# Performance work log

Hardware: AMD Instinct MI355X
Metric: run time of the kernel (lower is better)

## Reference

```python
import jax, jax.numpy as jnp
import numpy as np

V, DS, DF, H, NPASS = 32000, 64, 256, 8, 2
B, L, NB = 2, 1024, 512
EPS = 1e-5


def setup_inputs() -> dict:
    ks = jax.random.split(jax.random.key(0), 20)
    def n(k, shape, scale=0.02):
        return (scale * jax.random.normal(k, shape)).astype(jnp.float32)
    return {
        "token_ids": jax.random.randint(ks[0], (B, L), 0, V),
        "tok_mu": n(ks[1], (V, DS)),
        "tok_log_var": n(ks[2], (V, DS)),
        "tok_raw_alpha": n(ks[3], (V, 1), 1.0),
        "tok_features": n(ks[4], (V, DF)),
        "pos_mu": n(ks[5], (L, DS)),
        "qproj_w": n(ks[6], (H * DS, DS)),
        "qproj_b": jnp.zeros((H * DS,), jnp.float32),
        "hproj_w": n(ks[7], (DF, H * DF)),
        "hproj_b": jnp.zeros((DF,), jnp.float32),
        "mu_up_w": n(ks[8], (DS, 2 * DF)),
        "mu_up_b": jnp.zeros((DS,), jnp.float32),
        "agate_w": n(ks[9], (1, 2 * DF)),
        "agate_b": jnp.zeros((1,), jnp.float32),
        "ffn_w": n(ks[10], (DF, 2 * DF)),
        "ffn_b": jnp.zeros((DF,), jnp.float32),
        "ln_g": jnp.ones((DF,), jnp.float32),
        "ln_b": jnp.zeros((DF,), jnp.float32),
        "lm_w": n(ks[11], (V, DF)),
        "lm_b": jnp.zeros((V,), jnp.float32),
        "blob_mu": n(ks[12], (NB, DS)),
        "blob_lv": n(ks[13], (NB, DS)),
        "blob_ra": n(ks[14], (NB,), 1.0),
        "blob_f": n(ks[15], (NB, DF)),
        "bgate_w": n(ks[16], (1, 2 * DF)),
        "bgate_b": jnp.zeros((1,), jnp.float32),
    }


def _composite_weights(a):
    # front-to-back alpha compositing along last axis: w_j = a_j * prod_{k<j}(1-a_k)
    T = jnp.cumprod(1.0 - a, axis=-1)
    T_ex = jnp.concatenate([jnp.ones_like(T[..., :1]), T[..., :-1]], axis=-1)
    return a * T_ex, T[..., -1]


def _forward(token_ids, tok_mu, tok_log_var, tok_raw_alpha, tok_features, pos_mu,
             qproj_w, qproj_b, hproj_w, hproj_b, mu_up_w, mu_up_b, agate_w, agate_b,
             ffn_w, ffn_b, ln_g, ln_b, lm_w, lm_b, blob_mu, blob_lv, blob_ra, blob_f,
             bgate_w, bgate_b):
    Bc, Lc = token_ids.shape
    mu = tok_mu[token_ids] + pos_mu[:Lc][None]          # [B,L,DS]
    log_var = tok_log_var[token_ids]                     # [B,L,DS]
    alpha = jax.nn.sigmoid(tok_raw_alpha[token_ids][..., 0])  # [B,L]
    features = tok_features[token_ids]                   # [B,L,DF]

    # ---- blob query + blob render ----
    query = mu.mean(axis=1)                              # [B,DS]
    iv_b = jnp.exp(-blob_lv)                             # [NB,DS]
    d2b = (jnp.einsum('bd,nd->bn', query * query, iv_b)
           - 2.0 * jnp.einsum('bd,nd->bn', query, blob_mu * iv_b)
           + jnp.sum(blob_mu * blob_mu * iv_b, -1)[None])
    Kb = jnp.exp(-0.5 * d2b)                             # [B,NB]
    ab = jax.nn.sigmoid(blob_ra)[None] * Kb              # effective alpha
    wb, t_residual = _composite_weights(ab)
    blob_meaning = jnp.einsum('bn,nf->bf', wb, blob_f)   # [B,DF] (blob_proj = Identity)

    # ---- word meaning: multi-pass Gaussian causal render ----
    mask = jnp.tril(jnp.ones((Lc, Lc), jnp.float32))
    iv = jnp.exp(-log_var)                               # inv-variance, fixed across passes
    cur_mu, cur_alpha, cur_feat = mu, alpha, features
    meaning = None
    for p in range(NPASS):
        q = (cur_mu @ qproj_w.T + qproj_b).reshape(Bc, Lc, H, DS).transpose(0, 2, 1, 3)  # [B,H,L,DS]
        # squared Mahalanobis distance via three GEMM-style contractions (no [B,H,L,L,DS] tensor)
        d2 = (jnp.einsum('bhid,bjd->bhij', q * q, iv)
              - 2.0 * jnp.einsum('bhid,bjd->bhij', q, cur_mu * iv)
              + jnp.sum(cur_mu * cur_mu * iv, -1)[:, None, None, :])
        K = jnp.exp(-0.5 * d2)                           # [B,H,L,L]
        a = cur_alpha[:, None, None, :] * K * mask
        w, _ = _composite_weights(a)
        m = jnp.einsum('bhij,bjf->bhif', w, cur_feat)    # [B,H,L,DF]
        m_cat = m.transpose(0, 2, 1, 3).reshape(Bc, Lc, H * DF)
        meaning = m_cat @ hproj_w.T + hproj_b            # [B,L,DF] (dropout = eval/identity)
        if p < NPASS - 1:
            ctx = jnp.concatenate([cur_feat, meaning], axis=-1)  # [B,L,2DF]
            cur_mu = cur_mu + ctx @ mu_up_w.T + mu_up_b
            cur_alpha = cur_alpha * jax.nn.sigmoid(ctx @ agate_w.T + agate_b)[..., 0]
            cur_feat = cur_feat + ctx @ ffn_w.T + ffn_b

    # ---- blob gate fusion ----
    blob_exp = jnp.broadcast_to(blob_meaning[:, None, :], meaning.shape)
    gate = jax.nn.sigmoid(jnp.concatenate([blob_exp, meaning], -1) @ bgate_w.T + bgate_b)  # [B,L,1]
    t_res = t_residual[:, None, None]
    fused = (1.0 - t_res) * gate * blob_exp + t_res * meaning

    # ---- final layernorm + lm head ----
    mean = fused.mean(-1, keepdims=True)
    var = ((fused - mean) ** 2).mean(-1, keepdims=True)
    h = (fused - mean) * jax.lax.rsqrt(var + EPS) * ln_g + ln_b
    logits = h @ lm_w.T + lm_b                           # [B,L,V]
    return logits


def reference(token_ids, tok_mu, tok_log_var, tok_raw_alpha, tok_features, pos_mu,
              qproj_w, qproj_b, hproj_w, hproj_b, mu_up_w, mu_up_b, agate_w, agate_b,
              ffn_w, ffn_b, ln_g, ln_b, lm_w, lm_b, blob_mu, blob_lv, blob_ra, blob_f,
              bgate_w, bgate_b):
    return _forward(token_ids, tok_mu, tok_log_var, tok_raw_alpha, tok_features, pos_mu,
                    qproj_w, qproj_b, hproj_w, hproj_b, mu_up_w, mu_up_b, agate_w, agate_b,
                    ffn_w, ffn_b, ln_g, ln_b, lm_w, lm_b, blob_mu, blob_lv, blob_ra, blob_f,
                    bgate_w, bgate_b)
```

## Files before the change

### kernel.cpp

```cpp
#include <hip/hip_runtime.h>
#include <hip/hip_bf16.h>
#include <cstdint>
#include <cstddef>

#define V_   32000
#define DS_  64
#define DF_  256
#define H_   8
#define L_   1024
#define B_   2
#define NB_  512
#define BL_  2048
#define EPS_ 1e-5f

typedef unsigned short ushort_t;
typedef unsigned int uint_t;
typedef short bf16x8 __attribute__((ext_vector_type(8)));
typedef float f32x4 __attribute__((ext_vector_type(4)));
#define AS1 __attribute__((address_space(1)))
#define AS3 __attribute__((address_space(3)))

__device__ __forceinline__ float sigmoidf_(float x) { return 1.f / (1.f + __expf(-x)); }
__device__ __forceinline__ ushort_t f2bf(float x) {
    __hip_bfloat16 b = __float2bfloat16(x);
    return __builtin_bit_cast(ushort_t, b);
}
__device__ __forceinline__ uint_t packbf(float lo, float hi) {
    return ((uint_t)f2bf(hi) << 16) | (uint_t)f2bf(lo);
}
__device__ __forceinline__ float bflo(uint_t v) {
    return __builtin_bit_cast(float, v << 16);
}
__device__ __forceinline__ float bfhi(uint_t v) {
    return __builtin_bit_cast(float, v & 0xFFFF0000u);
}

__device__ __forceinline__ float block_reduce_sum(float v, float* red) {
    int t = threadIdx.x;
    red[t] = v;
    __syncthreads();
    for (int s = 128; s > 0; s >>= 1) {
        if (t < s) red[t] += red[t + s];
        __syncthreads();
    }
    float r = red[0];
    __syncthreads();
    return r;
}

#define NCVT_ 8720
#define NGA_  (NCVT_ + BL_)
#define NST_  (NGA_ + B_)
__global__ __launch_bounds__(256) void k_setup(
    const int* __restrict__ tok, const float* __restrict__ tok_mu,
    const float* __restrict__ tok_lv, const float* __restrict__ tok_ra,
    const float* __restrict__ tok_f, const float* __restrict__ pos_mu,
    const float* __restrict__ qproj_w, const float* __restrict__ mu_up_w,
    const float* __restrict__ mu_up_b, const float* __restrict__ ffn_w,
    const float* __restrict__ ffn_b, const float* __restrict__ agate_w,
    const float* __restrict__ agate_b, const float* __restrict__ hproj_w,
    const float* __restrict__ lm_w, const float* __restrict__ blob_mu,
    const float* __restrict__ blob_lv, const float* __restrict__ blob_ra,
    const float* __restrict__ blob_f,
    ushort_t* __restrict__ qpwbf, ushort_t* __restrict__ cwbf,
    ushort_t* __restrict__ hpwbf, ushort_t* __restrict__ wbf,
    float* __restrict__ cbias,
    float* __restrict__ mu, ushort_t* __restrict__ mub16,
    uint_t* __restrict__ muivP, float* __restrict__ alpha,
    float* __restrict__ feat, ushort_t* __restrict__ featb16,
    ushort_t* __restrict__ fTg, float* __restrict__ blobm,
    float* __restrict__ tres) {
    int blk = blockIdx.x;
    int t = threadIdx.x;
    if (blk < 32) {
        int i = (blk * 256 + t) * 4;
        float4 v = *reinterpret_cast<const float4*>(qproj_w + i);
        ushort4 o = {f2bf(v.x), f2bf(v.y), f2bf(v.z), f2bf(v.w)};
        *reinterpret_cast<ushort4*>(qpwbf + i) = o;
        return;
    }
    if (blk < 208) {
        int i = ((blk - 32) * 256 + t) * 4;
        int r = i >> 9, c = i & 511;
        float4 v = {0.f, 0.f, 0.f, 0.f};
        if (r < 64)        v = *reinterpret_cast<const float4*>(mu_up_w + r * 512 + c);
        else if (r < 320)  v = *reinterpret_cast<const float4*>(ffn_w + (r - 64) * 512 + c);
        else if (r == 320) v = *reinterpret_cast<const float4*>(agate_w + c);
        ushort4 o = {f2bf(v.x), f2bf(v.y), f2bf(v.z), f2bf(v.w)};
        *reinterpret_cast<ushort4*>(cwbf + i) = o;
        return;
    }
    if (blk < 720) {
        int i = ((blk - 208) * 256 + t) * 4;
        float4 v = *reinterpret_cast<const float4*>(hproj_w + i);
        ushort4 o = {f2bf(v.x), f2bf(v.y), f2bf(v.z), f2bf(v.w)};
        *reinterpret_cast<ushort4*>(hpwbf + i) = o;
        return;
    }
    if (blk < NCVT_) {
        int i = ((blk - 720) * 256 + t) * 4;
        float4 v = *reinterpret_cast<const float4*>(lm_w + i);
        ushort4 o = {f2bf(v.x), f2bf(v.y), f2bf(v.z), f2bf(v.w)};
        *reinterpret_cast<ushort4*>(wbf + i) = o;
        return;
    }
    if (blk < NGA_) {
        int row = blk - NCVT_;
        int l = row & (L_ - 1);
        int v = tok[row];
        if (t < DS_) {
            float m = tok_mu[(size_t)v * DS_ + t] + pos_mu[l * DS_ + t];
            mu[(size_t)row * DS_ + t] = m;
            mub16[(size_t)row * DS_ + t] = f2bf(m);
            float ivv = __expf(-tok_lv[(size_t)v * DS_ + t]);
            muivP[(size_t)t * BL_ + row] = packbf(m, ivv);
        }
        float fv = tok_f[(size_t)v * DF_ + t];
        feat[(size_t)row * DF_ + t] = fv;
        featb16[(size_t)row * DF_ + t] = f2bf(fv);
        int jb = (l >> 3) & 7, jr = l & 7;
        int jp = (l & ~63) | ((jb ^ (t & 7)) << 3) | jr;
        fTg[((size_t)((row >> 10) * DF_ + t) << 10) + jp] = f2bf(fv);
        if (t == 0) alpha[row] = sigmoidf_(tok_ra[v]);
        return;
    }
    if (blk < NST_) {
        __shared__ float red[256];
        __shared__ int stok[L_];
        __shared__ float sq[DS_];
        __shared__ float sa[NB_];
        __shared__ float sp[NB_];
        int b = blk - NGA_;
        for (int l = t; l < L_; l += 256) stok[l] = tok[b * L_ + l];
        __syncthreads();
        int d = t & 63, c = t >> 6;
        float s = 0.f;
        for (int l = c; l < L_; l += 4)
            s += tok_mu[(size_t)stok[l] * DS_ + d] + pos_mu[l * DS_ + d];
        red[t] = s;
        __syncthreads();
        if (c == 0)
            sq[d] = (red[d] + red[64 + d] + red[128 + d] + red[192 + d]) * (1.f / L_);
        __syncthreads();
        for (int n = t; n < NB_; n += 256) {
            float d2 = 0.f;
            for (int dd = 0; dd < DS_; ++dd) {
                float diff = sq[dd] - blob_mu[n * DS_ + dd];
                d2 += __expf(-blob_lv[n * DS_ + dd]) * diff * diff;
            }
            float a = sigmoidf_(blob_ra[n]) * __expf(-0.5f * d2);
            sa[n] = a;
            sp[n] = 1.f - a;
        }
        __syncthreads();
        int n0 = t, n1 = t + 256;
        for (int s2 = 1; s2 < NB_; s2 <<= 1) {
            float t0 = (n0 >= s2) ? sp[n0 - s2] : 1.f;
            float t1 = (n1 >= s2) ? sp[n1 - s2] : 1.f;
            __syncthreads();
            sp[n0] *= t0;
            sp[n1] *= t1;
            __syncthreads();
        }
        float w0 = sa[n0] * (n0 ? sp[n0 - 1] : 1.f);
        float w1 = sa[n1] * sp[n1 - 1];
        __syncthreads();
        sa[n0] = w0;
        sa[n1] = w1;
        if (t == 0) tres[b] = sp[NB_ - 1];
        __syncthreads();
        float acc = 0.f;
        for (int n = 0; n < NB_; ++n) acc += sa[n] * blob_f[n * DF_ + t];
        blobm[b * DF_ + t] = acc;
        return;
    }
    for (int idx = t; idx < 352; idx += 256) {
        float bv = 0.f;
        if (idx < 64) bv = mu_up_b[idx];
        else if (idx < 320) bv = ffn_b[idx - 64];
        else if (idx == 320) bv = agate_b[0];
        cbias[idx] = bv;
    }
}

__global__ __launch_bounds__(512) void k_attn5(
    const float* __restrict__ q, const uint_t* __restrict__ muivP,
    const float* __restrict__ alpha, const ushort_t* __restrict__ fTg,
    ushort_t* __restrict__ mcatb) {
    __shared__ __align__(16) uint_t smiu[64 * 64];
    __shared__ __align__(16) ushort_t sfT[256 * 64];
    __shared__ __align__(16) ushort_t sw16[16][72];
    __shared__ float sq[H_][64];
    __shared__ float sT[H_];
    int tid = threadIdx.x;
    int w = tid >> 6, lane = tid & 63;
    int bid = blockIdx.x;
    int b = bid >> 10, i = bid & (L_ - 1);
    int row = b * L_ + i;
    const int lr = lane & 15, q4 = lane >> 4;

    for (int k = tid; k < 16 * 72; k += 512) ((ushort_t*)sw16)[k] = 0;
    sq[w][lane] = q[(size_t)row * 512 + tid];

    float T = 1.f;
    f32x4 acc0 = {}, acc1 = {};

    for (int j0 = 0; j0 <= i; j0 += 64) {
        __syncthreads();
        if (j0 > 0) {
            bool alive = false;
            #pragma unroll
            for (int h = 0; h < H_; ++h) alive |= (sT[h] >= 1e-12f);
            if (!alive) break;
        }
        {
            const uint_t* src = muivP + b * L_ + j0;
            #pragma unroll
            for (int r = 0; r < 2; ++r) {
                int d = w * 8 + r * 4 + q4;
                const uint_t* gp = src + (size_t)d * BL_ + lr * 4;
                __builtin_amdgcn_global_load_lds((const AS1 uint_t*)gp,
                    (AS3 uint_t*)&smiu[(w * 8 + r * 4) * 64], 16, 0, 0);
            }
        }
        {
            #pragma unroll
            for (int it = 0; it < 4; ++it) {
                int c0 = w * 32 + it * 8;
                const ushort_t* gp = fTg +
                    ((size_t)(b * DF_ + c0 + (lane >> 3)) << 10) + j0 + (lane & 7) * 8;
                __builtin_amdgcn_global_load_lds((const AS1 uint_t*)gp,
                    (AS3 uint_t*)&sfT[c0 * 64], 16, 0, 0);
            }
        }
        __syncthreads();

        int jj = j0 + lane;
        float d2a = 0.f;
        #pragma unroll 8
        for (int d = 0; d < 64; ++d) {
            uint_t v = smiu[d * 64 + lane];
            float m = bflo(v), iv = bfhi(v);
            float diff = sq[w][d] - m;
            d2a = fmaf(iv * diff, diff, d2a);
        }
        float a = (jj <= i) ? alpha[b * L_ + jj] * __expf(-0.5f * d2a) : 0.f;

        float p = 1.f - a;
        #pragma unroll
        for (int s = 1; s < 64; s <<= 1) {
            float tt = __shfl_up(p, s, 64);
            if (lane >= s) p *= tt;
        }
        float Tex = __shfl_up(p, 1, 64);
        if (lane == 0) Tex = 1.f;
        sw16[w][lane] = f2bf(a * T * Tex);
        float Tch = __shfl(p, 63, 64);
        T *= Tch;
        if (lane == 0) sT[w] = T;
        __syncthreads();

        #pragma unroll
        for (int kk = 0; kk < 2; ++kk) {
            bf16x8 afr = *reinterpret_cast<const bf16x8*>(
                (const char*)sw16 + lr * 144 + kk * 64 + q4 * 16);
            {
                int c = (w * 2 + 0) * 16 + lr;
                int bo = c * 128 + ((kk * 64 + q4 * 16) ^ ((c & 7) << 4));
                bf16x8 bfr = *reinterpret_cast<const bf16x8*>((const char*)sfT + bo);
                acc0 = __builtin_amdgcn_mfma_f32_16x16x32_bf16(afr, bfr, acc0, 0, 0, 0);
            }
            {
                int c = (w * 2 + 1) * 16 + lr;
                int bo = c * 128 + ((kk * 64 + q4 * 16) ^ ((c & 7) << 4));
                bf16x8 bfr = *reinterpret_cast<const bf16x8*>((const char*)sfT + bo);
                acc1 = __builtin_amdgcn_mfma_f32_16x16x32_bf16(afr, bfr, acc1, 0, 0, 0);
            }
        }
    }
    if (q4 < 2) {
        #pragma unroll
        for (int r = 0; r < 4; ++r) {
            int h = q4 * 4 + r;
            int c0 = (w * 2 + 0) * 16 + lr;
            int c1 = (w * 2 + 1) * 16 + lr;
            mcatb[(size_t)row * 2048 + h * 256 + c0] = f2bf(acc0[r]);
            mcatb[(size_t)row * 2048 + h * 256 + c1] = f2bf(acc1[r]);
        }
    }
}

template <int BM, int BN, int BK, int WGM, int WGN, bool NTS, bool WB16>
__global__ __launch_bounds__(256) void gemm_mfma2(
    const ushort_t* __restrict__ A, const ushort_t* __restrict__ A2, int K1,
    int strideA, const ushort_t* __restrict__ W, const float* __restrict__ bias,
    float* __restrict__ C, ushort_t* __restrict__ Cb, int M, int N, int K) {
    constexpr int WMF = BM / WGM / 16;
    constexpr int WNF = BN / WGN / 16;
    constexpr int KK  = BK / 32;
    constexpr int AHALF = BM * BK;
    constexpr int BHALF = BN * BK;
    constexpr int STAGE_B = 2 * (AHALF + BHALF) * 2;
    constexpr int EPI_B = BM * BN * 4;
    constexpr int SMEM_B = STAGE_B > EPI_B ? STAGE_B : EPI_B;
    __shared__ __align__(16) char smem[SMEM_B];
    ushort_t* As = (ushort_t*)smem;
    ushort_t* Bs = (ushort_t*)(smem + 2 * AHALF * 2);

    const int tid = threadIdx.x;
    const int wave = tid >> 6, lane = tid & 63;
    const int m0 = blockIdx.x * BM, n0 = blockIdx.y * BN;
    const int wr = wave / WGN, wc = wave % WGN;
    const int lr = lane & 15;
    const int q4 = lane >> 4;

    f32x4 acc[WMF][WNF] = {};

    auto stage = [&](int buf, int t) {
        const int k0g = t * BK;
        const ushort_t* Abase = (A2 != nullptr && k0g >= K1) ? A2 : A;
        const int kof = (A2 != nullptr && k0g >= K1) ? k0g - K1 : k0g;
        ushort_t* Ad = As + buf * AHALF;
        #pragma unroll
        for (int it = 0; it < (BM * BK / 8) / 256; ++it) {
            int cbase = it * 256 + wave * 64;
            int c = cbase + lane;
            int r = c & (BM - 1), c8 = c / BM;
            const ushort_t* gp = Abase + (size_t)(m0 + r) * strideA + kof + c8 * 8;
            __builtin_amdgcn_global_load_lds((const AS1 uint_t*)gp,
                                             (AS3 uint_t*)(Ad + cbase * 8), 16, 0, 0);
        }
        ushort_t* Bd = Bs + buf * BHALF;
        #pragma unroll
        for (int it = 0; it < (BN * BK / 8) / 256; ++it) {
            int cbase = it * 256 + wave * 64;
            int c = cbase + lane;
            int r = c & (BN - 1), c8 = c / BN;
            const ushort_t* gp = W + (size_t)(n0 + r) * K + k0g + c8 * 8;
            __builtin_amdgcn_global_load_lds((const AS1 uint_t*)gp,
                                             (AS3 uint_t*)(Bd + cbase * 8), 16, 0, 0);
        }
    };

    const int nsteps = K / BK;
    stage(0, 0);
    __syncthreads();
    for (int t = 0; t < nsteps; ++t) {
        const int cur = t & 1;
        if (t + 1 < nsteps) stage(cur ^ 1, t + 1);
        const ushort_t* Ab = As + cur * AHALF;
        const ushort_t* Bb = Bs + cur * BHALF;
        bf16x8 af[WMF][KK], bfr[WNF][KK];
        #pragma unroll
        for (int mi = 0; mi < WMF; ++mi)
            #pragma unroll
            for (int kk = 0; kk < KK; ++kk)
                af[mi][kk] = *reinterpret_cast<const bf16x8*>(
                    &Ab[((kk * 4 + q4) * BM + wr * (BM / WGM) + mi * 16 + lr) * 8]);
        #pragma unroll
        for (int ni = 0; ni < WNF; ++ni)
            #pragma unroll
            for (int kk = 0; kk < KK; ++kk)
                bfr[ni][kk] = *reinterpret_cast<const bf16x8*>(
                    &Bb[((kk * 4 + q4) * BN + wc * (BN / WGN) + ni * 16 + lr) * 8]);
        #pragma unroll
        for (int kk = 0; kk < KK; ++kk)
            #pragma unroll
            for (int mi = 0; mi < WMF; ++mi)
                #pragma unroll
                for (int ni = 0; ni < WNF; ++ni)
                    acc[mi][ni] = __builtin_amdgcn_mfma_f32_16x16x32_bf16(
                        af[mi][kk], bfr[ni][kk], acc[mi][ni], 0, 0, 0);
        __syncthreads();
    }

    float* tile = (float*)smem;
    #pragma unroll
    for (int mi = 0; mi < WMF; ++mi)
        #pragma unroll
        for (int ni = 0; ni < WNF; ++ni) {
            int col = wc * (BN / WGN) + ni * 16 + lr;
            float bv = bias[n0 + col];
            #pragma unroll
            for (int j = 0; j < 4; ++j) {
                int r2 = wr * (BM / WGM) + mi * 16 + q4 * 4 + j;
                tile[r2 * BN + col] = acc[mi][ni][j] + bv;
            }
        }
    __syncthreads();
    constexpr int EV = (BM * BN / 4) / 256;
    #pragma unroll
    for (int e = 0; e < EV; ++e) {
        int idx = e * 256 + tid;
        int r = idx / (BN / 4), c4 = idx % (BN / 4);
        f32x4 v = reinterpret_cast<const f32x4*>(tile)[idx];
        f32x4* dst = reinterpret_cast<f32x4*>(&C[(size_t)(m0 + r) * N + n0 + c4 * 4]);
        if (NTS) __builtin_nontemporal_store(v, dst);
        else *dst = v;
        if (WB16) {
            ushort4 ob = {f2bf(v[0]), f2bf(v[1]), f2bf(v[2]), f2bf(v[3])};
            *reinterpret_cast<ushort4*>(&Cb[(size_t)(m0 + r) * N + n0 + c4 * 4]) = ob;
        }
    }
}

__global__ __launch_bounds__(256) void k_apply(
    const float* __restrict__ dctx, float* __restrict__ mu,
    ushort_t* __restrict__ mub16, uint_t* __restrict__ muivP,
    float* __restrict__ alpha, float* __restrict__ feat,
    ushort_t* __restrict__ featb16, ushort_t* __restrict__ fTg) {
    int row = blockIdx.x, t = threadIdx.x;
    int l = row & (L_ - 1);
    const float* dr = dctx + (size_t)row * 352;
    if (t == 0) alpha[row] *= sigmoidf_(dr[320]);
    if (t < DS_) {
        float m = mu[(size_t)row * DS_ + t] + dr[t];
        mu[(size_t)row * DS_ + t] = m;
        mub16[(size_t)row * DS_ + t] = f2bf(m);
        uint_t v = muivP[(size_t)t * BL_ + row];
        muivP[(size_t)t * BL_ + row] = (v & 0xFFFF0000u) | (uint_t)f2bf(m);
    }
    float fn = feat[(size_t)row * DF_ + t] + dr[64 + t];
    feat[(size_t)row * DF_ + t] = fn;
    featb16[(size_t)row * DF_ + t] = f2bf(fn);
    int jb = (l >> 3) & 7, jr = l & 7;
    int jp = (l & ~63) | ((jb ^ (t & 7)) << 3) | jr;
    fTg[((size_t)((row >> 10) * DF_ + t) << 10) + jp] = f2bf(fn);
}

__global__ __launch_bounds__(256) void k_fused_ln(
    const float* __restrict__ meaning, const float* __restrict__ blobm,
    const float* __restrict__ tres, const float* __restrict__ bgw,
    const float* __restrict__ bgb, const float* __restrict__ ln_g,
    const float* __restrict__ ln_b, ushort_t* __restrict__ houtb) {
    __shared__ float red[256];
    int row = blockIdx.x, t = threadIdx.x;
    int b = row >> 10;
    float m = meaning[(size_t)row * DF_ + t];
    float be = blobm[b * DF_ + t];
    float tr = tres[b];
    float gsum = block_reduce_sum(be * bgw[t] + m * bgw[256 + t], red);
    float gate = sigmoidf_(gsum + bgb[0]);
    float f = (1.f - tr) * gate * be + tr * m;
    float mean = block_reduce_sum(f, red) * (1.f / DF_);
    float d = f - mean;
    float var = block_reduce_sum(d * d, red) * (1.f / DF_);
    houtb[(size_t)row * DF_ + t] = f2bf(d * rsqrtf(var + EPS_) * ln_g[t] + ln_b[t]);
}

extern "C" void kernel_launch(void* const* d_in, const int* in_sizes, int n_in,
                              void* d_out, int out_size, void* d_ws, size_t ws_size,
                              hipStream_t stream) {
    const int*   tok      = (const int*)d_in[0];
    const float* tok_mu   = (const float*)d_in[1];
    const float* tok_lv   = (const float*)d_in[2];
    const float* tok_ra   = (const float*)d_in[3];
    const float* tok_f    = (const float*)d_in[4];
    const float* pos_mu   = (const float*)d_in[5];
    const float* qproj_w  = (const float*)d_in[6];
    const float* qproj_b  = (const float*)d_in[7];
    const float* hproj_w  = (const float*)d_in[8];
    const float* hproj_b  = (const float*)d_in[9];
    const float* mu_up_w  = (const float*)d_in[10];
    const float* mu_up_b  = (const float*)d_in[11];
    const float* agate_w  = (const float*)d_in[12];
    const float* agate_b  = (const float*)d_in[13];
    const float* ffn_w    = (const float*)d_in[14];
    const float* ffn_b    = (const float*)d_in[15];
    const float* ln_g     = (const float*)d_in[16];
    const float* ln_b     = (const float*)d_in[17];
    const float* lm_w     = (const float*)d_in[18];
    const float* lm_b     = (const float*)d_in[19];
    const float* blob_mu  = (const float*)d_in[20];
    const float* blob_lv  = (const float*)d_in[21];
    const float* blob_ra  = (const float*)d_in[22];
    const float* blob_f   = (const float*)d_in[23];
    const float* bgate_w  = (const float*)d_in[24];
    const float* bgate_b  = (const float*)d_in[25];
    float* out = (float*)d_out;

    float* ws = (float*)d_ws;
    float* mu      = ws;
    float* alpha   = mu + BL_ * DS_;
    float* feat    = alpha + BL_;
    float* blobm   = feat + BL_ * DF_;
    float* tres    = blobm + B_ * DF_;
    float* q       = tres + 64;
    float* meaning = q + BL_ * 512;
    float* dctx    = meaning + BL_ * DF_;
    float* cbias   = dctx + (size_t)BL_ * 352;
    uint_t* muivP  = (uint_t*)(cbias + 384);
    ushort_t* fTg   = (ushort_t*)(muivP + (size_t)DS_ * BL_);
    ushort_t* mub16 = fTg + (size_t)B_ * DF_ * L_;
    ushort_t* featb16 = mub16 + (size_t)BL_ * DS_;
    ushort_t* meanb16 = featb16 + (size_t)BL_ * DF_;
    ushort_t* mcatb = meanb16 + (size_t)BL_ * DF_;
    ushort_t* hbufb = mcatb + (size_t)BL_ * 2048;
    ushort_t* wbf   = hbufb + (size_t)BL_ * DF_;
    ushort_t* hpwbf = wbf + (size_t)V_ * DF_;
    ushort_t* qpwbf = hpwbf + (size_t)DF_ * 2048;
    ushort_t* cwbf  = qpwbf + (size_t)512 * 64;

    k_setup<<<NST_ + 1, 256, 0, stream>>>(
        tok, tok_mu, tok_lv, tok_ra, tok_f, pos_mu,
        qproj_w, mu_up_w, mu_up_b, ffn_w, ffn_b, agate_w, agate_b,
        hproj_w, lm_w, blob_mu, blob_lv, blob_ra, blob_f,
        qpwbf, cwbf, hpwbf, wbf, cbias,
        mu, mub16, muivP, alpha, feat, featb16, fTg, blobm, tres);

    for (int p = 0; p < 2; ++p) {
        gemm_mfma2<32, 32, 64, 2, 2, false, false>
            <<<dim3(BL_ / 32, 512 / 32), 256, 0, stream>>>(
            mub16, nullptr, 0, DS_, qpwbf, qproj_b, q, nullptr, BL_, 512, DS_);
        k_attn5<<<BL_, 512, 0, stream>>>(q, muivP, alpha, fTg, mcatb);
        if (p == 0) {
            gemm_mfma2<32, 32, 128, 2, 2, false, true>
                <<<dim3(BL_ / 32, DF_ / 32), 256, 0, stream>>>(
                mcatb, nullptr, 0, H_ * DF_, hpwbf, hproj_b, meaning, meanb16,
                BL_, DF_, H_ * DF_);
            gemm_mfma2<32, 32, 128, 2, 2, false, false>
                <<<dim3(BL_ / 32, 352 / 32), 256, 0, stream>>>(
                featb16, meanb16, DF_, DF_, cwbf, cbias, dctx, nullptr,
                BL_, 352, 512);
            k_apply<<<BL_, 256, 0, stream>>>(dctx, mu, mub16, muivP, alpha,
                                             feat, featb16, fTg);
        } else {
            gemm_mfma2<32, 32, 128, 2, 2, false, false>
                <<<dim3(BL_ / 32, DF_ / 32), 256, 0, stream>>>(
                mcatb, nullptr, 0, H_ * DF_, hpwbf, hproj_b, meaning, nullptr,
                BL_, DF_, H_ * DF_);
        }
    }

    k_fused_ln<<<BL_, 256, 0, stream>>>(meaning, blobm, tres, bgate_w, bgate_b,
                                        ln_g, ln_b, hbufb);
    gemm_mfma2<128, 128, 64, 2, 2, true, false>
        <<<dim3(BL_ / 128, V_ / 128), 256, 0, stream>>>(
        hbufb, nullptr, 0, DF_, wbf, lm_b, out, nullptr, BL_, V_, DF_);
}
```

Measured before the change: 312.0 us.

## Process two query rows per attention block, coarsen setup conversion, shrink LM-head tile

The attention kernel now handles two adjacent query rows per block, so the loaded mu/inv-var and feature tiles are shared and the 16 MFMA A-rows are fully used instead of half. The setup kernel converts four float4 chunks per thread, which cuts the number of conversion blocks by four. The LM-head GEMM tile changes from 128x128 to 64x128 to launch more workgroups. The costs are a second per-row scan, more registers, and the block only exits early once both rows are saturated.

```diff
diff --git a/kernel.cpp b/kernel.cpp
--- a/kernel.cpp
+++ b/kernel.cpp
@@ -48,7 +48,7 @@
     return r;
 }
 
-#define NCVT_ 8720
+#define NCVT_ 2180
 #define NGA_  (NCVT_ + BL_)
 #define NST_  (NGA_ + B_)
 __global__ __launch_bounds__(256) void k_setup(
@@ -72,36 +72,27 @@
     float* __restrict__ tres) {
     int blk = blockIdx.x;
     int t = threadIdx.x;
-    if (blk < 32) {
-        int i = (blk * 256 + t) * 4;
-        float4 v = *reinterpret_cast<const float4*>(qproj_w + i);
-        ushort4 o = {f2bf(v.x), f2bf(v.y), f2bf(v.z), f2bf(v.w)};
-        *reinterpret_cast<ushort4*>(qpwbf + i) = o;
-        return;
-    }
-    if (blk < 208) {
-        int i = ((blk - 32) * 256 + t) * 4;
-        int r = i >> 9, c = i & 511;
-        float4 v = {0.f, 0.f, 0.f, 0.f};
-        if (r < 64)        v = *reinterpret_cast<const float4*>(mu_up_w + r * 512 + c);
-        else if (r < 320)  v = *reinterpret_cast<const float4*>(ffn_w + (r - 64) * 512 + c);
-        else if (r == 320) v = *reinterpret_cast<const float4*>(agate_w + c);
-        ushort4 o = {f2bf(v.x), f2bf(v.y), f2bf(v.z), f2bf(v.w)};
-        *reinterpret_cast<ushort4*>(cwbf + i) = o;
-        return;
-    }
-    if (blk < 720) {
-        int i = ((blk - 208) * 256 + t) * 4;
-        float4 v = *reinterpret_cast<const float4*>(hproj_w + i);
-        ushort4 o = {f2bf(v.x), f2bf(v.y), f2bf(v.z), f2bf(v.w)};
-        *reinterpret_cast<ushort4*>(hpwbf + i) = o;
-        return;
-    }
     if (blk < NCVT_) {
-        int i = ((blk - 720) * 256 + t) * 4;
-        float4 v = *reinterpret_cast<const float4*>(lm_w + i);
-        ushort4 o = {f2bf(v.x), f2bf(v.y), f2bf(v.z), f2bf(v.w)};
-        *reinterpret_cast<ushort4*>(wbf + i) = o;
+        const float* s = nullptr; ushort_t* dd; int base; bool cw = false;
+        if (blk < 8)        { s = qproj_w; dd = qpwbf; base = blk; }
+        else if (blk < 52)  { dd = cwbf; base = blk - 8; cw = true; }
+        else if (blk < 180) { s = hproj_w; dd = hpwbf; base = blk - 52; }
+        else                { s = lm_w; dd = wbf; base = blk - 180; }
+        #pragma unroll
+        for (int k = 0; k < 4; ++k) {
+            int i = base * 4096 + k * 1024 + t * 4;
+            float4 v = {0.f, 0.f, 0.f, 0.f};
+            if (cw) {
+                int r = i >> 9, c = i & 511;
+                if (r < 64)        v = *reinterpret_cast<const float4*>(mu_up_w + r * 512 + c);
+                else if (r < 320)  v = *reinterpret_cast<const float4*>(ffn_w + (r - 64) * 512 + c);
+                else if (r == 320) v = *reinterpret_cast<const float4*>(agate_w + c);
+            } else {
+                v = *reinterpret_cast<const float4*>(s + i);
+            }
+            ushort4 o = {f2bf(v.x), f2bf(v.y), f2bf(v.z), f2bf(v.w)};
+            *reinterpret_cast<ushort4*>(dd + i) = o;
+        }
         return;
     }
     if (blk < NGA_) {
@@ -183,34 +174,35 @@
     }
 }
 
-__global__ __launch_bounds__(512) void k_attn5(
+__global__ __launch_bounds__(512) void k_attn7(
     const float* __restrict__ q, const uint_t* __restrict__ muivP,
     const float* __restrict__ alpha, const ushort_t* __restrict__ fTg,
     ushort_t* __restrict__ mcatb) {
     __shared__ __align__(16) uint_t smiu[64 * 64];
     __shared__ __align__(16) ushort_t sfT[256 * 64];
     __shared__ __align__(16) ushort_t sw16[16][72];
-    __shared__ float sq[H_][64];
-    __shared__ float sT[H_];
+    __shared__ float sqA[512], sqB[512];
+    __shared__ float sT[16];
     int tid = threadIdx.x;
     int w = tid >> 6, lane = tid & 63;
     int bid = blockIdx.x;
-    int b = bid >> 10, i = bid & (L_ - 1);
-    int row = b * L_ + i;
+    int b = bid >> 9;
+    int i0 = (bid & 511) * 2, i1 = i0 + 1;
+    int row0 = b * L_ + i0;
     const int lr = lane & 15, q4 = lane >> 4;
 
-    for (int k = tid; k < 16 * 72; k += 512) ((ushort_t*)sw16)[k] = 0;
-    sq[w][lane] = q[(size_t)row * 512 + tid];
-
-    float T = 1.f;
+    sqA[tid] = q[(size_t)row0 * 512 + tid];
+    sqB[tid] = q[(size_t)(row0 + 1) * 512 + tid];
+
+    float T0 = 1.f, T1 = 1.f;
     f32x4 acc0 = {}, acc1 = {};
 
-    for (int j0 = 0; j0 <= i; j0 += 64) {
+    for (int j0 = 0; j0 <= i1; j0 += 64) {
         __syncthreads();
         if (j0 > 0) {
             bool alive = false;
             #pragma unroll
-            for (int h = 0; h < H_; ++h) alive |= (sT[h] >= 1e-12f);
+            for (int h = 0; h < 16; ++h) alive |= (sT[h] >= 1e-12f);
             if (!alive) break;
         }
         {
@@ -236,17 +228,22 @@
         __syncthreads();
 
         int jj = j0 + lane;
-        float d2a = 0.f;
+        int jc = jj <= i1 ? jj : i1;
+        float alv = alpha[b * L_ + jc];
+        float d20 = 0.f, d21 = 0.f;
         #pragma unroll 8
         for (int d = 0; d < 64; ++d) {
             uint_t v = smiu[d * 64 + lane];
             float m = bflo(v), iv = bfhi(v);
-            float diff = sq[w][d] - m;
-            d2a = fmaf(iv * diff, diff, d2a);
-        }
-        float a = (jj <= i) ? alpha[b * L_ + jj] * __expf(-0.5f * d2a) : 0.f;
-
-        float p = 1.f - a;
+            float f0 = sqA[w * 64 + d] - m;
+            float f1 = sqB[w * 64 + d] - m;
+            d20 = fmaf(iv * f0, f0, d20);
+            d21 = fmaf(iv * f1, f1, d21);
+        }
+        float a0 = (jj <= i0) ? alv * __expf(-0.5f * d20) : 0.f;
+        float a1 = (jj <= i1) ? alv * __expf(-0.5f * d21) : 0.f;
+
+        float p = 1.f - a0;
         #pragma unroll
         for (int s = 1; s < 64; s <<= 1) {
             float tt = __shfl_up(p, s, 64);
@@ -254,10 +251,21 @@
         }
         float Tex = __shfl_up(p, 1, 64);
         if (lane == 0) Tex = 1.f;
-        sw16[w][lane] = f2bf(a * T * Tex);
-        float Tch = __shfl(p, 63, 64);
-        T *= Tch;
-        if (lane == 0) sT[w] = T;
+        sw16[w][lane] = f2bf(a0 * T0 * Tex);
+        T0 *= __shfl(p, 63, 64);
+
+        p = 1.f - a1;
+        #pragma unroll
+        for (int s = 1; s < 64; s <<= 1) {
+            float tt = __shfl_up(p, s, 64);
+            if (lane >= s) p *= tt;
+        }
+        Tex = __shfl_up(p, 1, 64);
+        if (lane == 0) Tex = 1.f;
+        sw16[w + 8][lane] = f2bf(a1 * T1 * Tex);
+        T1 *= __shfl(p, 63, 64);
+
+        if (lane == 0) { sT[w] = T0; sT[w + 8] = T1; }
         __syncthreads();
 
         #pragma unroll
@@ -278,15 +286,13 @@
             }
         }
     }
-    if (q4 < 2) {
-        #pragma unroll
-        for (int r = 0; r < 4; ++r) {
-            int h = q4 * 4 + r;
-            int c0 = (w * 2 + 0) * 16 + lr;
-            int c1 = (w * 2 + 1) * 16 + lr;
-            mcatb[(size_t)row * 2048 + h * 256 + c0] = f2bf(acc0[r]);
-            mcatb[(size_t)row * 2048 + h * 256 + c1] = f2bf(acc1[r]);
-        }
+    #pragma unroll
+    for (int j = 0; j < 4; ++j) {
+        int r = q4 * 4 + j;
+        int h = r & 7, par = r >> 3;
+        size_t rw = (size_t)(row0 + par) * 2048 + h * 256;
+        mcatb[rw + (w * 2 + 0) * 16 + lr] = f2bf(acc0[j]);
+        mcatb[rw + (w * 2 + 1) * 16 + lr] = f2bf(acc1[j]);
     }
 }
 
@@ -512,7 +518,7 @@
         gemm_mfma2<32, 32, 64, 2, 2, false, false>
             <<<dim3(BL_ / 32, 512 / 32), 256, 0, stream>>>(
             mub16, nullptr, 0, DS_, qpwbf, qproj_b, q, nullptr, BL_, 512, DS_);
-        k_attn5<<<BL_, 512, 0, stream>>>(q, muivP, alpha, fTg, mcatb);
+        k_attn7<<<B_ * L_ / 2, 512, 0, stream>>>(q, muivP, alpha, fTg, mcatb);
         if (p == 0) {
             gemm_mfma2<32, 32, 128, 2, 2, false, true>
                 <<<dim3(BL_ / 32, DF_ / 32), 256, 0, stream>>>(
@@ -534,7 +540,7 @@
 
     k_fused_ln<<<BL_, 256, 0, stream>>>(meaning, blobm, tres, bgate_w, bgate_b,
                                         ln_g, ln_b, hbufb);
-    gemm_mfma2<128, 128, 64, 2, 2, true, false>
-        <<<dim3(BL_ / 128, V_ / 128), 256, 0, stream>>>(
+    gemm_mfma2<64, 128, 64, 2, 2, true, false>
+        <<<dim3(BL_ / 64, V_ / 128), 256, 0, stream>>>(
         hbufb, nullptr, 0, DF_, wbf, lm_b, out, nullptr, BL_, V_, DF_);
 }
```

After: 319.9 us. +2.5%, slower.
